# Performance work log

Hardware: AMD Instinct MI355X
Metric: run time of the kernel (lower is better)

The kernel has to match this reference:

```python
import jax, jax.numpy as jnp
import numpy as np
import math

GRID = 14  # coords run 1..13 -> 13x13 spatial grid
Z = math.exp(math.log(2.0 * math.pi) + 1.0)
EPS = 1e-06

def setup_inputs() -> dict:
    key = jax.random.key(0)
    B, C = 256, 1024
    x = jax.random.normal(key, (B, GRID - 1, GRID - 1, C), dtype=jnp.float32)
    return {"feature_input": x}

def reference(feature_input) -> jnp.ndarray:
    B, H, W, C = feature_input.shape
    f = jax.nn.softmax(feature_input, axis=3)  # softmax over channel dim (dim=3)
    coords = jnp.arange(1, GRID, dtype=jnp.float32)  # [13]
    xv = coords[:, None]  # varies along spatial axis 0 (torch meshgrid 'ij')
    yv = coords[None, :]  # varies along spatial axis 1
    s = f.sum(axis=(1, 2)) + EPS  # [B, C] per-slice mass
    # soft-argmax centroids, [B, C]
    mx = (xv[None, :, :, None] * f).sum(axis=(1, 2)) / s
    my = (yv[None, :, :, None] * f).sum(axis=(1, 2)) / s
    # weighted variances, normalized by 169 and the per-slice mass
    dx2 = (xv[None, :, :, None] - mx[:, None, None, :]) ** 2
    dy2 = (yv[None, :, :, None] - my[:, None, None, :]) ** 2
    x_var = (dx2 * f).sum(axis=(1, 2)) / 169.0 / s
    y_var = (dy2 * f).sum(axis=(1, 2)) / 169.0 / s
    det_xy = (x_var + y_var) ** 2 * Z  # [B, C]
    return det_xy.sum() / B / C
```

## Files before the change

kernel.cpp:

```cpp
#include <hip/hip_runtime.h>

#ifndef __has_builtin
#define __has_builtin(x) 0
#endif

__device__ __forceinline__ float fast_exp2(float x) {
#if __has_builtin(__builtin_amdgcn_exp2f)
    return __builtin_amdgcn_exp2f(x);
#else
    return exp2f(x);
#endif
}

__device__ __forceinline__ float wave_sum_dpp(float x) {
    int v;
    v = __builtin_amdgcn_update_dpp(0, __float_as_int(x), 0x111, 0xf, 0xf, true);
    x += __int_as_float(v);
    v = __builtin_amdgcn_update_dpp(0, __float_as_int(x), 0x112, 0xf, 0xf, true);
    x += __int_as_float(v);
    v = __builtin_amdgcn_update_dpp(0, __float_as_int(x), 0x114, 0xf, 0xf, true);
    x += __int_as_float(v);
    v = __builtin_amdgcn_update_dpp(0, __float_as_int(x), 0x118, 0xf, 0xf, true);
    x += __int_as_float(v);
    v = __builtin_amdgcn_update_dpp(0, __float_as_int(x), 0x142, 0xa, 0xf, false);
    x += __int_as_float(v);
    v = __builtin_amdgcn_update_dpp(0, __float_as_int(x), 0x143, 0xc, 0xf, false);
    x += __int_as_float(v);
    return x;
}

constexpr int   kB      = 256;
constexpr int   kC      = 1024;
constexpr int   kG      = 13;
constexpr int   kP      = kG * kG;
constexpr int   kParts  = 4;
constexpr int   kMaxPP  = 43;
constexpr float kEps    = 1e-6f;
constexpr float kZ      = 17.079468445347132f;
constexpr float kLog2e  = 1.4426950408889634f;
constexpr float kInv169 = 1.0f / 169.0f;
constexpr float kScale  = 1.0f / (256.0f * 1024.0f);

__global__ __launch_bounds__(1024, 4)
void part_stats_kernel(const float* __restrict__ x, float* __restrict__ ws)
{
    __shared__ float sP[kMaxPP * 16];
    __shared__ float sInvD[kMaxPP];

    const int tid   = threadIdx.x;
    const int lane  = tid & 63;
    const int wid   = tid >> 6;
    const int b     = blockIdx.x >> 2;
    const int part  = blockIdx.x & 3;
    const int start = part * 42;
    const bool full = (part == 3);

    const float* __restrict__ xc = x + (size_t)b * kP * kC + (size_t)start * kC + tid;

    float e[kMaxPP];
    #pragma unroll
    for (int i = 0; i < kMaxPP; ++i)
        e[i] = xc[(size_t)i * kC];

    #pragma unroll
    for (int i = 0; i < kMaxPP; ++i)
        e[i] = fast_exp2(e[i] * kLog2e);

    if (!full) e[42] = 0.0f;

    #pragma unroll
    for (int i = 0; i < kMaxPP; ++i) {
        const float s = wave_sum_dpp(e[i]);
        if (lane == 63) sP[i * 16 + wid] = s;
    }
    __syncthreads();

    if (tid < kMaxPP) {
        float d = 0.f;
        #pragma unroll
        for (int w = 0; w < 16; ++w)
            d += sP[tid * 16 + w];
        sInvD[tid] = 1.0f / (d + 1e-30f);
    }
    __syncthreads();

    float S0 = 0.f, S1x = 0.f, S1y = 0.f, S2x = 0.f, S2y = 0.f;
    #pragma unroll
    for (int i = 0; i < kMaxPP; ++i) {
        const float f  = e[i] * sInvD[i];
        const int   p  = start + i;
        const int   h  = p / kG;
        const int   w  = p - h * kG;
        const float fx = (float)(h + 1);
        const float fy = (float)(w + 1);
        S0  += f;
        S1x  = fmaf(fx,      f, S1x);
        S1y  = fmaf(fy,      f, S1y);
        S2x  = fmaf(fx * fx, f, S2x);
        S2y  = fmaf(fy * fy, f, S2y);
    }

    float* __restrict__ o = ws + (((size_t)part * kB + b) * 5) * kC + tid;
    o[0 * kC] = S0;
    o[1 * kC] = S1x;
    o[2 * kC] = S1y;
    o[3 * kC] = S2x;
    o[4 * kC] = S2y;
}

__global__ __launch_bounds__(1024, 4)
void combine_kernel(const float* __restrict__ ws, float* __restrict__ out)
{
    __shared__ float sred[16];

    const int tid  = threadIdx.x;
    const int lane = tid & 63;
    const int wid  = tid >> 6;
    const int b    = blockIdx.x;

    float S0 = 0.f, S1x = 0.f, S1y = 0.f, S2x = 0.f, S2y = 0.f;
    #pragma unroll
    for (int part = 0; part < kParts; ++part) {
        const float* __restrict__ o = ws + (((size_t)part * kB + b) * 5) * kC + tid;
        S0  += o[0 * kC];
        S1x += o[1 * kC];
        S1y += o[2 * kC];
        S2x += o[3 * kC];
        S2y += o[4 * kC];
    }

    const float s   = S0 + kEps;
    const float is  = 1.0f / s;
    const float mx  = S1x * is;
    const float my  = S1y * is;
    const float nx  = S2x - mx * (2.0f * S1x - mx * S0);
    const float ny  = S2y - my * (2.0f * S1y - my * S0);
    const float t   = (nx + ny) * is * kInv169;
    float det = t * t * kZ;

    #pragma unroll
    for (int m = 1; m < 64; m <<= 1)
        det += __shfl_xor(det, m);

    if (lane == 0) sred[wid] = det;
    __syncthreads();
    if (wid == 0) {
        float v = (lane < 16) ? sred[lane] : 0.0f;
        #pragma unroll
        for (int m = 1; m < 16; m <<= 1)
            v += __shfl_xor(v, m);
        if (lane == 0) atomicAdd(out, v * kScale);
    }
}

extern "C" void kernel_launch(void* const* d_in, const int* in_sizes, int n_in,
                              void* d_out, int out_size, void* d_ws, size_t ws_size,
                              hipStream_t stream)
{
    const float* x   = (const float*)d_in[0];
    float*       out = (float*)d_out;
    float*       ws  = (float*)d_ws;

    hipMemsetAsync(out, 0, sizeof(float) * (size_t)out_size, stream);
    part_stats_kernel<<<dim3(kB * kParts), dim3(1024), 0, stream>>>(x, ws);
    combine_kernel  <<<dim3(kB),           dim3(1024), 0, stream>>>(ws, out);
}
```

Baseline: 260.3 us.

## Fuse part-stats and combine kernels into one per-batch kernel

Measured after the change: 248.6 us (median of 2 runs). 4.5% less time.

```diff
diff --git a/kernel.cpp b/kernel.cpp
--- a/kernel.cpp
+++ b/kernel.cpp
@@ -42,75 +42,10 @@
 constexpr float kScale  = 1.0f / (256.0f * 1024.0f);
 
 __global__ __launch_bounds__(1024, 4)
-void part_stats_kernel(const float* __restrict__ x, float* __restrict__ ws)
+void fused_kernel(const float* __restrict__ x, float* __restrict__ out)
 {
     __shared__ float sP[kMaxPP * 16];
     __shared__ float sInvD[kMaxPP];
-
-    const int tid   = threadIdx.x;
-    const int lane  = tid & 63;
-    const int wid   = tid >> 6;
-    const int b     = blockIdx.x >> 2;
-    const int part  = blockIdx.x & 3;
-    const int start = part * 42;
-    const bool full = (part == 3);
-
-    const float* __restrict__ xc = x + (size_t)b * kP * kC + (size_t)start * kC + tid;
-
-    float e[kMaxPP];
-    #pragma unroll
-    for (int i = 0; i < kMaxPP; ++i)
-        e[i] = xc[(size_t)i * kC];
-
-    #pragma unroll
-    for (int i = 0; i < kMaxPP; ++i)
-        e[i] = fast_exp2(e[i] * kLog2e);
-
-    if (!full) e[42] = 0.0f;
-
-    #pragma unroll
-    for (int i = 0; i < kMaxPP; ++i) {
-        const float s = wave_sum_dpp(e[i]);
-        if (lane == 63) sP[i * 16 + wid] = s;
-    }
-    __syncthreads();
-
-    if (tid < kMaxPP) {
-        float d = 0.f;
-        #pragma unroll
-        for (int w = 0; w < 16; ++w)
-            d += sP[tid * 16 + w];
-        sInvD[tid] = 1.0f / (d + 1e-30f);
-    }
-    __syncthreads();
-
-    float S0 = 0.f, S1x = 0.f, S1y = 0.f, S2x = 0.f, S2y = 0.f;
-    #pragma unroll
-    for (int i = 0; i < kMaxPP; ++i) {
-        const float f  = e[i] * sInvD[i];
-        const int   p  = start + i;
-        const int   h  = p / kG;
-        const int   w  = p - h * kG;
-        const float fx = (float)(h + 1);
-        const float fy = (float)(w + 1);
-        S0  += f;
-        S1x  = fmaf(fx,      f, S1x);
-        S1y  = fmaf(fy,      f, S1y);
-        S2x  = fmaf(fx * fx, f, S2x);
-        S2y  = fmaf(fy * fy, f, S2y);
-    }
-
-    float* __restrict__ o = ws + (((size_t)part * kB + b) * 5) * kC + tid;
-    o[0 * kC] = S0;
-    o[1 * kC] = S1x;
-    o[2 * kC] = S1y;
-    o[3 * kC] = S2x;
-    o[4 * kC] = S2y;
-}
-
-__global__ __launch_bounds__(1024, 4)
-void combine_kernel(const float* __restrict__ ws, float* __restrict__ out)
-{
     __shared__ float sred[16];
 
     const int tid  = threadIdx.x;
@@ -119,14 +54,56 @@
     const int b    = blockIdx.x;
 
     float S0 = 0.f, S1x = 0.f, S1y = 0.f, S2x = 0.f, S2y = 0.f;
-    #pragma unroll
+
     for (int part = 0; part < kParts; ++part) {
-        const float* __restrict__ o = ws + (((size_t)part * kB + b) * 5) * kC + tid;
-        S0  += o[0 * kC];
-        S1x += o[1 * kC];
-        S1y += o[2 * kC];
-        S2x += o[3 * kC];
-        S2y += o[4 * kC];
+        const int  start = part * 42;
+        const bool full  = (part == 3);
+
+        const float* __restrict__ xc =
+            x + (size_t)b * kP * kC + (size_t)start * kC + tid;
+
+        float e[kMaxPP];
+        #pragma unroll
+        for (int i = 0; i < kMaxPP; ++i)
+            e[i] = xc[(size_t)i * kC];
+
+        #pragma unroll
+        for (int i = 0; i < kMaxPP; ++i)
+            e[i] = fast_exp2(e[i] * kLog2e);
+
+        if (!full) e[42] = 0.0f;
+
+        #pragma unroll
+        for (int i = 0; i < kMaxPP; ++i) {
+            const float s = wave_sum_dpp(e[i]);
+            if (lane == 63) sP[i * 16 + wid] = s;
+        }
+        __syncthreads();
+
+        if (tid < kMaxPP) {
+            float d = 0.f;
+            #pragma unroll
+            for (int w = 0; w < 16; ++w)
+                d += sP[tid * 16 + w];
+            sInvD[tid] = 1.0f / (d + 1e-30f);
+        }
+        __syncthreads();
+
+        int h = 3 * part;
+        int w = 3 * part;
+        #pragma unroll
+        for (int i = 0; i < kMaxPP; ++i) {
+            const float f  = e[i] * sInvD[i];
+            const float fx = (float)(h + 1);
+            const float fy = (float)(w + 1);
+            S0  += f;
+            S1x  = fmaf(fx,      f, S1x);
+            S1y  = fmaf(fy,      f, S1y);
+            S2x  = fmaf(fx * fx, f, S2x);
+            S2y  = fmaf(fy * fy, f, S2y);
+            ++w;
+            if (w == kG) { w = 0; ++h; }
+        }
     }
 
     const float s   = S0 + kEps;
@@ -159,9 +136,7 @@
 {
     const float* x   = (const float*)d_in[0];
     float*       out = (float*)d_out;
-    float*       ws  = (float*)d_ws;
 
     hipMemsetAsync(out, 0, sizeof(float) * (size_t)out_size, stream);
-    part_stats_kernel<<<dim3(kB * kParts), dim3(1024), 0, stream>>>(x, ws);
-    combine_kernel  <<<dim3(kB),           dim3(1024), 0, stream>>>(ws, out);
+    fused_kernel<<<dim3(kB), dim3(1024), 0, stream>>>(x, out);
 }
```
